# Performance work log

Measured on AMD Instinct MI355X. Metric: run time of the kernel, lower is better.

Reference implementation:

```python
import jax, jax.numpy as jnp
import numpy as np

EMBED_DIM = 1024
B, S = 4, 2048


def setup_inputs() -> dict:
    key = jax.random.key(0)
    ks = jax.random.split(key, 7)
    D = EMBED_DIM
    lim = 1.0 / np.sqrt(D)  # torch nn.Linear default init range
    inp = {
        "input": jax.random.normal(ks[0], (B, S, D), dtype=jnp.float32),
        "Wq": jax.random.uniform(ks[1], (D, D), jnp.float32, -lim, lim),
        "bq": jax.random.uniform(ks[2], (D,), jnp.float32, -lim, lim),
        "Wk": jax.random.uniform(ks[3], (D, D), jnp.float32, -lim, lim),
        "bk": jax.random.uniform(ks[4], (D,), jnp.float32, -lim, lim),
        "Wv": jax.random.uniform(ks[5], (D, D), jnp.float32, -lim, lim),
        "bv": jax.random.uniform(ks[6], (D,), jnp.float32, -lim, lim),
    }
    return inp


def reference(input, Wq, bq, Wk, bk, Wv, bv):
    # Linear layers: x @ W^T + b (torch convention: W is [out, in])
    q = jnp.einsum("bsd,ed->bse", input, Wq) + bq
    k = jnp.einsum("bsd,ed->bse", input, Wk) + bk
    v = jnp.einsum("bsd,ed->bse", input, Wv) + bv
    scale = 1.0 / jnp.sqrt(jnp.float32(EMBED_DIM))
    # [B, S, S] similarity matrix (unfused, matches original)
    similarity = jnp.einsum("bqd,bkd->bqk", q, k) * scale
    attention = jax.nn.softmax(similarity, axis=-1)
    return jnp.einsum("bqk,bkd->bqd", attention, v)
```

## Files before the change

kernel.cpp:

```cpp
#include <hip/hip_runtime.h>


typedef unsigned short ushort_t;
typedef __bf16 bf16x8 __attribute__((ext_vector_type(8)));
typedef float f32x4 __attribute__((ext_vector_type(4)));

__device__ __forceinline__ unsigned short f2bf(float f) {
  unsigned u = __builtin_bit_cast(unsigned, f);
  u += 0x7fffu + ((u >> 16) & 1u);
  return (unsigned short)(u >> 16);
}

template<int BM, int MODE, int RX, int RY>
__global__ __launch_bounds__(512, 1)
void gemm8p(const ushort_t* __restrict__ A, long long sAz, int lda,
            const ushort_t* __restrict__ Bm, long long sBz, int ldb,
            void* __restrict__ C0, void* __restrict__ C1, void* __restrict__ C2,
            long long sCz, int ldc, int K, float scale, const float* __restrict__ bias)
{
  constexpr int MF  = BM / 32;
  constexpr int MH  = MF / 2;
  constexpr int AH  = (BM / 2) * 64;
  constexpr int BH  = 128 * 64;
  constexpr int BUF = 2 * AH + 2 * BH;
  constexpr int SWA = AH / 4096;
  constexpr int BPR = RX * RY;
  __shared__ ushort_t lds_[2 * BUF] __attribute__((aligned(16)));

  const int gx = gridDim.x;
  const int lin = blockIdx.y * gx + blockIdx.x;
  const int xcd = lin & 7, s = lin >> 3;
  const int chunk = s / BPR, idx = s % BPR;
  const int rect = chunk * 8 + xcd;
  const int nrx = gx / RX;
  const int bx = (rect % nrx) * RX + (idx % RX);
  const int by = (rect / nrx) * RY + (idx / RX);

  const int z = blockIdx.z;
  const ushort_t* Ab = A  + (long long)z * sAz + (long long)by * BM  * lda;
  const ushort_t* Bb = Bm + (long long)z * sBz + (long long)bx * 256 * ldb;

  const int tid = threadIdx.x, wid = tid >> 6, lane = tid & 63;
  const int wr = wid >> 2, wc = wid & 3;
  const int l15 = lane & 15;
  const int kx0 = (((lane >> 4) + 0) ^ (l15 & 7)) * 8;
  const int kx1 = (((lane >> 4) + 4) ^ (l15 & 7)) * 8;
  const int srow = lane >> 3;
  const int scol = ((lane & 7) ^ (srow & 7)) * 8;

  auto stgA = [&](int q, int h, int t) {
#pragma unroll
    for (int j = 0; j < SWA; ++j) {
      const ushort_t* g = Ab + (long long)(h * (BM / 2) + wid * (8 * SWA) + j * 8 + srow) * lda
                             + t * 64 + scol;
      __builtin_amdgcn_global_load_lds(
          (const __attribute__((address_space(1))) void*)g,
          (__attribute__((address_space(3))) void*)
            (&lds_[q * BUF + h * AH + (wid * (64 * SWA) + j * 64) * 8]),
          16, 0, 0);
    }
  };
  auto stgB = [&](int q, int h, int t) {
#pragma unroll
    for (int j = 0; j < 2; ++j) {
      const ushort_t* g = Bb + (long long)(h * 128 + wid * 16 + j * 8 + srow) * ldb
                             + t * 64 + scol;
      __builtin_amdgcn_global_load_lds(
          (const __attribute__((address_space(1))) void*)g,
          (__attribute__((address_space(3))) void*)
            (&lds_[q * BUF + 2 * AH + h * BH + (wid * 128 + j * 64) * 8]),
          16, 0, 0);
    }
  };

  f32x4 acc[MF][4];
#pragma unroll
  for (int m = 0; m < MF; ++m)
#pragma unroll
    for (int n = 0; n < 4; ++n)
#pragma unroll
      for (int j = 0; j < 4; ++j) acc[m][n][j] = 0.f;

  stgA(0, 0, 0); stgA(0, 1, 0);
  stgB(0, 0, 0); stgB(0, 1, 0);
  stgA(1, 0, 1); stgA(1, 1, 1);
  if constexpr (SWA == 2) asm volatile("s_waitcnt vmcnt(4)" ::: "memory");
  else                    asm volatile("s_waitcnt vmcnt(2)" ::: "memory");
  __builtin_amdgcn_s_barrier();

  const int NT = K >> 6;

  if constexpr (MF == 4) {
    bf16x8 a0[4], a1[4], bf[4];
    for (int t = 0; t < NT; ++t) {
      const int q = t & 1;
      const ushort_t* Al = &lds_[q * BUF + wr * AH];
      const ushort_t* Bl = &lds_[q * BUF + 2 * AH + (wc >> 1) * BH + (wc & 1) * 4096];

#pragma unroll
      for (int m = 0; m < 4; ++m) a0[m] = *(const bf16x8*)(Al + (m * 16 + l15) * 64 + kx0);
#pragma unroll
      for (int n = 0; n < 4; ++n) bf[n] = *(const bf16x8*)(Bl + (n * 16 + l15) * 64 + kx0);
#pragma unroll
      for (int m = 0; m < 4; ++m) a1[m] = *(const bf16x8*)(Al + (m * 16 + l15) * 64 + kx1);
      __builtin_amdgcn_sched_barrier(0);
      if (t + 1 < NT) { stgB(q ^ 1, 0, t + 1); stgB(q ^ 1, 1, t + 1); }
      __builtin_amdgcn_s_barrier();
      __builtin_amdgcn_s_setprio(1);
#pragma unroll
      for (int m = 0; m < 4; ++m)
#pragma unroll
        for (int n = 0; n < 4; ++n)
          acc[m][n] = __builtin_amdgcn_mfma_f32_16x16x32_bf16(a0[m], bf[n], acc[m][n], 0, 0, 0);
      __builtin_amdgcn_s_setprio(0);
      __builtin_amdgcn_s_barrier();

#pragma unroll
      for (int n = 0; n < 4; ++n) bf[n] = *(const bf16x8*)(Bl + (n * 16 + l15) * 64 + kx1);
      __builtin_amdgcn_sched_barrier(0);
      if (t + 2 < NT) { stgA(q, 0, t + 2); stgA(q, 1, t + 2); }
      __builtin_amdgcn_s_barrier();
      __builtin_amdgcn_s_setprio(1);
#pragma unroll
      for (int m = 0; m < 4; ++m)
#pragma unroll
        for (int n = 0; n < 4; ++n)
          acc[m][n] = __builtin_amdgcn_mfma_f32_16x16x32_bf16(a1[m], bf[n], acc[m][n], 0, 0, 0);
      __builtin_amdgcn_s_setprio(0);
      if (t < NT - 2)       asm volatile("s_waitcnt vmcnt(2)" ::: "memory");
      else if (t == NT - 2) asm volatile("s_waitcnt vmcnt(0)" ::: "memory");
      __builtin_amdgcn_s_barrier();
    }
  } else {
    bf16x8 af[MH], bf[4];
    for (int t = 0; t < NT; ++t) {
      const int q = t & 1;
      const ushort_t* Al = &lds_[q * BUF + wr * AH];
      const ushort_t* Bl = &lds_[q * BUF + 2 * AH + (wc >> 1) * BH + (wc & 1) * 4096];

#pragma unroll
      for (int n = 0; n < 4; ++n) bf[n] = *(const bf16x8*)(Bl + (n * 16 + l15) * 64 + kx0);
#pragma unroll
      for (int m = 0; m < MH; ++m) af[m] = *(const bf16x8*)(Al + (m * 16 + l15) * 64 + kx0);
      if (t + 1 < NT) stgB(q ^ 1, 0, t + 1);
      __builtin_amdgcn_s_barrier();
      __builtin_amdgcn_s_setprio(1);
#pragma unroll
      for (int m = 0; m < MH; ++m)
#pragma unroll
        for (int n = 0; n < 4; ++n)
          acc[m][n] = __builtin_amdgcn_mfma_f32_16x16x32_bf16(af[m], bf[n], acc[m][n], 0, 0, 0);
      __builtin_amdgcn_s_setprio(0);
      __builtin_amdgcn_s_barrier();

#pragma unroll
      for (int m = 0; m < MH; ++m) af[m] = *(const bf16x8*)(Al + ((MH + m) * 16 + l15) * 64 + kx0);
      if (t + 1 < NT) stgB(q ^ 1, 1, t + 1);
      __builtin_amdgcn_s_barrier();
      __builtin_amdgcn_s_setprio(1);
#pragma unroll
      for (int m = 0; m < MH; ++m)
#pragma unroll
        for (int n = 0; n < 4; ++n)
          acc[MH + m][n] = __builtin_amdgcn_mfma_f32_16x16x32_bf16(af[m], bf[n], acc[MH + m][n], 0, 0, 0);
      __builtin_amdgcn_s_setprio(0);
      __builtin_amdgcn_s_barrier();

#pragma unroll
      for (int n = 0; n < 4; ++n) bf[n] = *(const bf16x8*)(Bl + (n * 16 + l15) * 64 + kx1);
#pragma unroll
      for (int m = 0; m < MH; ++m) af[m] = *(const bf16x8*)(Al + (m * 16 + l15) * 64 + kx1);
      __builtin_amdgcn_s_barrier();
      __builtin_amdgcn_s_setprio(1);
#pragma unroll
      for (int m = 0; m < MH; ++m)
#pragma unroll
        for (int n = 0; n < 4; ++n)
          acc[m][n] = __builtin_amdgcn_mfma_f32_16x16x32_bf16(af[m], bf[n], acc[m][n], 0, 0, 0);
      __builtin_amdgcn_s_setprio(0);
      __builtin_amdgcn_s_barrier();

#pragma unroll
      for (int m = 0; m < MH; ++m) af[m] = *(const bf16x8*)(Al + ((MH + m) * 16 + l15) * 64 + kx1);
      __builtin_amdgcn_sched_barrier(0);
      if (t + 2 < NT) { stgA(q, 0, t + 2); stgA(q, 1, t + 2); }
      __builtin_amdgcn_s_barrier();
      __builtin_amdgcn_s_setprio(1);
#pragma unroll
      for (int m = 0; m < MH; ++m)
#pragma unroll
        for (int n = 0; n < 4; ++n)
          acc[MH + m][n] = __builtin_amdgcn_mfma_f32_16x16x32_bf16(af[m], bf[n], acc[MH + m][n], 0, 0, 0);
      __builtin_amdgcn_s_setprio(0);
      if (t < NT - 2)       asm volatile("s_waitcnt vmcnt(4)" ::: "memory");
      else if (t == NT - 2) asm volatile("s_waitcnt vmcnt(0)" ::: "memory");
      __builtin_amdgcn_s_barrier();
    }
  }

  const int r4 = (lane >> 4) * 4;
  const long long crow0 = (long long)by * BM + wr * (BM / 2);
  const int ccol0 = bx * 256 + wc * 64;
#pragma unroll
  for (int n = 0; n < 4; ++n) {
    const int cg = ccol0 + n * 16 + l15;
    const float badd = bias ? bias[cg] : 0.f;
    ushort_t* outp = (ushort_t*)C0;
    int col = cg;
    if constexpr (MODE == 2) {
      const int sel = cg >> 10;
      col = cg & 1023;
      outp = (ushort_t*)(sel == 0 ? C0 : (sel == 1 ? C1 : C2));
    }
#pragma unroll
    for (int m = 0; m < MF; ++m)
#pragma unroll
      for (int j = 0; j < 4; ++j) {
        const long long rg = crow0 + m * 16 + r4 + j;
        const float v = acc[m][n][j] * scale + badd;
        if constexpr (MODE == 0)
          ((float*)C0)[(long long)z * sCz + rg * ldc + cg] = v;
        else if constexpr (MODE == 1)
          ((ushort_t*)C0)[(long long)z * sCz + rg * ldc + cg] = f2bf(v);
        else
          outp[rg * 1024 + col] = f2bf(v);
      }
  }
}

__global__ __launch_bounds__(256)
void cast_f32_bf16(const float* __restrict__ in, ushort_t* __restrict__ out, long long n)
{
  long long i = ((long long)blockIdx.x * blockDim.x + threadIdx.x) * 4;
  const long long stride = (long long)gridDim.x * blockDim.x * 4;
  for (; i < n; i += stride) {
    const float4 v = *(const float4*)&in[i];
    ushort4 o;
    o.x = f2bf(v.x); o.y = f2bf(v.y); o.z = f2bf(v.z); o.w = f2bf(v.w);
    *(ushort4*)&out[i] = o;
  }
}

__global__ __launch_bounds__(256)
void prep_w(const float* __restrict__ Wq, const float* __restrict__ Wk,
            const float* __restrict__ Wv, const float* __restrict__ bq,
            const float* __restrict__ bk, const float* __restrict__ bv,
            ushort_t* __restrict__ w3, float* __restrict__ bcat)
{
  const int which = blockIdx.x >> 10;
  const float* W = (which == 0) ? Wq : (which == 1) ? Wk : Wv;
  const long long i = ((long long)(blockIdx.x & 1023) * 256 + threadIdx.x) * 4;
  const float4 v = *(const float4*)&W[i];
  ushort4 o;
  o.x = f2bf(v.x); o.y = f2bf(v.y); o.z = f2bf(v.z); o.w = f2bf(v.w);
  *(ushort4*)&w3[(long long)which * 1024 * 1024 + i] = o;
  const int g = blockIdx.x * 256 + threadIdx.x;
  if (g < 3072) bcat[g] = (g < 1024) ? bq[g] : (g < 2048) ? bk[g - 1024] : bv[g - 2048];
}

__global__ __launch_bounds__(256)
void transpose_bf16(const ushort_t* __restrict__ in, ushort_t* __restrict__ out,
                    int rows, int cols, int ldIn, long long sIn, long long sOut)
{
  __shared__ ushort_t t[64][65];
  in  += (long long)blockIdx.z * sIn;
  out += (long long)blockIdx.z * sOut;
  const int r0 = blockIdx.y * 64;
  const int c0 = blockIdx.x * 64;
  const int tx = threadIdx.x & 15, ty = threadIdx.x >> 4;
#pragma unroll
  for (int r = 0; r < 4; ++r) {
    const ushort4 v = *(const ushort4*)&in[(long long)(r0 + ty * 4 + r) * ldIn + c0 + tx * 4];
    t[ty * 4 + r][tx * 4 + 0] = v.x;
    t[ty * 4 + r][tx * 4 + 1] = v.y;
    t[ty * 4 + r][tx * 4 + 2] = v.z;
    t[ty * 4 + r][tx * 4 + 3] = v.w;
  }
  __syncthreads();
#pragma unroll
  for (int r = 0; r < 4; ++r) {
    const int d = ty * 4 + r;
    ushort4 v;
    v.x = t[tx * 4 + 0][d];
    v.y = t[tx * 4 + 1][d];
    v.z = t[tx * 4 + 2][d];
    v.w = t[tx * 4 + 3][d];
    *(ushort4*)&out[(long long)(c0 + d) * rows + r0 + tx * 4] = v;
  }
}

__global__ __launch_bounds__(256)
void softmax2048(const float* __restrict__ Sc, ushort_t* __restrict__ P)
{
  const long long row = blockIdx.x;
  const float* s = Sc + row * 2048;
  const int tid = threadIdx.x;
  const int wave = tid >> 6, lane = tid & 63;

  const float4 a = *(const float4*)&s[tid * 4];
  const float4 b = *(const float4*)&s[1024 + tid * 4];
  float m = fmaxf(fmaxf(fmaxf(a.x, a.y), fmaxf(a.z, a.w)),
                  fmaxf(fmaxf(b.x, b.y), fmaxf(b.z, b.w)));
#pragma unroll
  for (int off = 32; off > 0; off >>= 1) m = fmaxf(m, __shfl_xor(m, off));
  __shared__ float redm[4], reds[4];
  if (lane == 0) redm[wave] = m;
  __syncthreads();
  m = fmaxf(fmaxf(redm[0], redm[1]), fmaxf(redm[2], redm[3]));

  float e[8];
  e[0] = __expf(a.x - m); e[1] = __expf(a.y - m); e[2] = __expf(a.z - m); e[3] = __expf(a.w - m);
  e[4] = __expf(b.x - m); e[5] = __expf(b.y - m); e[6] = __expf(b.z - m); e[7] = __expf(b.w - m);
  float sum = ((e[0] + e[1]) + (e[2] + e[3])) + ((e[4] + e[5]) + (e[6] + e[7]));
#pragma unroll
  for (int off = 32; off > 0; off >>= 1) sum += __shfl_xor(sum, off);
  if (lane == 0) reds[wave] = sum;
  __syncthreads();
  sum = (reds[0] + reds[1]) + (reds[2] + reds[3]);
  const float inv = 1.0f / sum;

  ushort4 o;
  o.x = f2bf(e[0] * inv); o.y = f2bf(e[1] * inv); o.z = f2bf(e[2] * inv); o.w = f2bf(e[3] * inv);
  *(ushort4*)&P[row * 2048 + tid * 4] = o;
  o.x = f2bf(e[4] * inv); o.y = f2bf(e[5] * inv); o.z = f2bf(e[6] * inv); o.w = f2bf(e[7] * inv);
  *(ushort4*)&P[row * 2048 + 1024 + tid * 4] = o;
}

extern "C" void kernel_launch(void* const* d_in, const int* in_sizes, int n_in,
                              void* d_out, int out_size, void* d_ws, size_t ws_size,
                              hipStream_t stream)
{
  constexpr int B = 4, S = 2048, D = 1024;
  constexpr long long MT = (long long)B * S;
  constexpr long long SD = (long long)S * D;
  constexpr long long SS = (long long)S * S;

  const float* x  = (const float*)d_in[0];
  const float* Wq = (const float*)d_in[1];
  const float* bq = (const float*)d_in[2];
  const float* Wk = (const float*)d_in[3];
  const float* bk = (const float*)d_in[4];
  const float* Wv = (const float*)d_in[5];
  const float* bv = (const float*)d_in[6];
  float* out = (float*)d_out;

  char* base = (char*)d_ws;
  ushort_t* q      = (ushort_t*)(base);
  ushort_t* k      = (ushort_t*)(base + 16777216);
  ushort_t* vt     = (ushort_t*)(base + 33554432);
  float*    scores = (float*)   (base + 50331648);
  ushort_t* P      = (ushort_t*)(base + 117440512);
  ushort_t* vplain = (ushort_t*)(base + 150994944);
  ushort_t* xb     = (ushort_t*)(base + 50331648);
  ushort_t* w3     = (ushort_t*)(base + 67108864);
  float*    bcat   = (float*)   (base + 73400320);

  cast_f32_bf16<<<2048, 256, 0, stream>>>(x, xb, MT * D);
  prep_w<<<3072, 256, 0, stream>>>(Wq, Wk, Wv, bq, bk, bv, w3, bcat);

  gemm8p<128, 2, 4, 8><<<dim3(12, 64, 1), 512, 0, stream>>>(
      xb, 0, D, w3, 0, D, q, k, vplain, 0, 1024, D, 1.f, bcat);

  transpose_bf16<<<dim3(16, 32, 4), 256, 0, stream>>>(
      vplain, vt, S, D, 1024, SD, SD);

  gemm8p<256, 0, 4, 2><<<dim3(8, 8, 4), 512, 0, stream>>>(
      q, SD, D, k, SD, D, scores, nullptr, nullptr, SS, S, D, 0.03125f, nullptr);

  softmax2048<<<MT, 256, 0, stream>>>(scores, P);

  gemm8p<128, 0, 2, 4><<<dim3(4, 16, 4), 512, 0, stream>>>(
      P, SS, S, vt, (long long)D * S, S, out, nullptr, nullptr, SD, D, S, 1.f, nullptr);
}
```

Measured before the change: 185.0 us.

## Fuse V transpose into QKV GEMM epilogue and use 128x128 tiles with higher occupancy

Splits the templated GEMM into a 128x128-tile kernel (launch bounds allowing 4 blocks per CU) and a dedicated 256x256 kernel for the QK^T scores. The QKV projection GEMM now writes the V slice directly in transposed layout from its epilogue, which removes the separate transpose kernel and the extra round trip through memory. The QKV and PV GEMMs move to smaller tiles with more blocks, trading per-block reuse for better occupancy and wave coverage. The transposed V stores are 8-byte strided writes, which may coalesce worse than the old row-major stores.

Result: faster. 175.8 us (-5.0%).

```diff
diff --git a/kernel.cpp b/kernel.cpp
--- a/kernel.cpp
+++ b/kernel.cpp
@@ -11,22 +11,18 @@
   return (unsigned short)(u >> 16);
 }
 
-template<int BM, int MODE, int RX, int RY>
-__global__ __launch_bounds__(512, 1)
-void gemm8p(const ushort_t* __restrict__ A, long long sAz, int lda,
-            const ushort_t* __restrict__ Bm, long long sBz, int ldb,
-            void* __restrict__ C0, void* __restrict__ C1, void* __restrict__ C2,
-            long long sCz, int ldc, int K, float scale, const float* __restrict__ bias)
-{
-  constexpr int MF  = BM / 32;
-  constexpr int MH  = MF / 2;
-  constexpr int AH  = (BM / 2) * 64;
-  constexpr int BH  = 128 * 64;
-  constexpr int BUF = 2 * AH + 2 * BH;
-  constexpr int SWA = AH / 4096;
+template<int MODE, int RX, int RY>
+__global__ __launch_bounds__(512, 4)
+void gemm128(const ushort_t* __restrict__ A, long long sAz, int lda,
+             const ushort_t* __restrict__ Bm, long long sBz, int ldb,
+             void* __restrict__ C0, void* __restrict__ C1, void* __restrict__ C2,
+             long long sCz, int ldc, int K, float scale, const float* __restrict__ bias)
+{
+  constexpr int SLOT = 8192;
+  constexpr int BUF  = 2 * SLOT;
+  __shared__ ushort_t lds_[2 * BUF] __attribute__((aligned(16)));
+
   constexpr int BPR = RX * RY;
-  __shared__ ushort_t lds_[2 * BUF] __attribute__((aligned(16)));
-
   const int gx = gridDim.x;
   const int lin = blockIdx.y * gx + blockIdx.x;
   const int xcd = lin & 7, s = lin >> 3;
@@ -37,8 +33,8 @@
   const int by = (rect / nrx) * RY + (idx / RX);
 
   const int z = blockIdx.z;
-  const ushort_t* Ab = A  + (long long)z * sAz + (long long)by * BM  * lda;
-  const ushort_t* Bb = Bm + (long long)z * sBz + (long long)bx * 256 * ldb;
+  const ushort_t* Ab = A  + (long long)z * sAz + (long long)by * 128 * lda;
+  const ushort_t* Bb = Bm + (long long)z * sBz + (long long)bx * 128 * ldb;
 
   const int tid = threadIdx.x, wid = tid >> 6, lane = tid & 63;
   const int wr = wid >> 2, wc = wid & 3;
@@ -48,15 +44,165 @@
   const int srow = lane >> 3;
   const int scol = ((lane & 7) ^ (srow & 7)) * 8;
 
+  auto stg = [&](int mat, int q, int t) {
+    const ushort_t* g0 = (mat == 0 ? Ab : Bb);
+    const int ld = (mat == 0 ? lda : ldb);
+#pragma unroll
+    for (int j = 0; j < 2; ++j) {
+      const ushort_t* g = g0 + (long long)(j * 64 + wid * 8 + srow) * ld + t * 64 + scol;
+      __builtin_amdgcn_global_load_lds(
+          (const __attribute__((address_space(1))) void*)g,
+          (__attribute__((address_space(3))) void*)
+            (&lds_[q * BUF + mat * SLOT + (j * 64 + wid * 8) * 64]),
+          16, 0, 0);
+    }
+  };
+
+  f32x4 acc[4][2];
+#pragma unroll
+  for (int m = 0; m < 4; ++m)
+#pragma unroll
+    for (int n = 0; n < 2; ++n)
+#pragma unroll
+      for (int j = 0; j < 4; ++j) acc[m][n][j] = 0.f;
+
+  stg(0, 0, 0); stg(1, 0, 0); stg(0, 1, 1);
+  asm volatile("s_waitcnt vmcnt(2)" ::: "memory");
+  __builtin_amdgcn_s_barrier();
+
+  const int NT = K >> 6;
+  bf16x8 a0[4], a1[4], bf[2];
+
+  for (int t = 0; t < NT; ++t) {
+    const int q = t & 1;
+    const ushort_t* Al = &lds_[q * BUF] + wr * 64 * 64;
+    const ushort_t* Bl = &lds_[q * BUF + SLOT] + wc * 32 * 64;
+
+#pragma unroll
+    for (int m = 0; m < 4; ++m) a0[m] = *(const bf16x8*)(Al + (m * 16 + l15) * 64 + kx0);
+#pragma unroll
+    for (int n = 0; n < 2; ++n) bf[n] = *(const bf16x8*)(Bl + (n * 16 + l15) * 64 + kx0);
+#pragma unroll
+    for (int m = 0; m < 4; ++m) a1[m] = *(const bf16x8*)(Al + (m * 16 + l15) * 64 + kx1);
+    __builtin_amdgcn_sched_barrier(0);
+    if (t + 1 < NT) stg(1, q ^ 1, t + 1);
+    __builtin_amdgcn_s_barrier();
+    __builtin_amdgcn_s_setprio(1);
+#pragma unroll
+    for (int m = 0; m < 4; ++m)
+#pragma unroll
+      for (int n = 0; n < 2; ++n)
+        acc[m][n] = __builtin_amdgcn_mfma_f32_16x16x32_bf16(a0[m], bf[n], acc[m][n], 0, 0, 0);
+    __builtin_amdgcn_s_setprio(0);
+    __builtin_amdgcn_s_barrier();
+
+#pragma unroll
+    for (int n = 0; n < 2; ++n) bf[n] = *(const bf16x8*)(Bl + (n * 16 + l15) * 64 + kx1);
+    __builtin_amdgcn_sched_barrier(0);
+    if (t + 2 < NT) stg(0, q, t + 2);
+    __builtin_amdgcn_s_barrier();
+    __builtin_amdgcn_s_setprio(1);
+#pragma unroll
+    for (int m = 0; m < 4; ++m)
+#pragma unroll
+      for (int n = 0; n < 2; ++n)
+        acc[m][n] = __builtin_amdgcn_mfma_f32_16x16x32_bf16(a1[m], bf[n], acc[m][n], 0, 0, 0);
+    __builtin_amdgcn_s_setprio(0);
+    if (t < NT - 2)       asm volatile("s_waitcnt vmcnt(2)" ::: "memory");
+    else if (t == NT - 2) asm volatile("s_waitcnt vmcnt(0)" ::: "memory");
+    __builtin_amdgcn_s_barrier();
+  }
+
+  const int r4 = (lane >> 4) * 4;
+  const long long crow0 = (long long)by * 128 + wr * 64;
+  const int ccol0 = bx * 128 + wc * 32;
+
+  if constexpr (MODE == 0) {
+#pragma unroll
+    for (int n = 0; n < 2; ++n) {
+      const int cg = ccol0 + n * 16 + l15;
+#pragma unroll
+      for (int m = 0; m < 4; ++m)
+#pragma unroll
+        for (int j = 0; j < 4; ++j) {
+          const long long rg = crow0 + m * 16 + r4 + j;
+          ((float*)C0)[(long long)z * sCz + rg * ldc + cg] = acc[m][n][j] * scale;
+        }
+    }
+  } else {
+    const int sel = ccol0 >> 10;
+#pragma unroll
+    for (int n = 0; n < 2; ++n) {
+      const int cg = ccol0 + n * 16 + l15;
+      const int col = cg & 1023;
+      const float badd = bias[cg];
+      if (sel < 2) {
+        ushort_t* outp = (ushort_t*)(sel == 0 ? C0 : C1);
+#pragma unroll
+        for (int m = 0; m < 4; ++m)
+#pragma unroll
+          for (int j = 0; j < 4; ++j) {
+            const long long rg = crow0 + m * 16 + r4 + j;
+            outp[rg * 1024 + col] = f2bf(acc[m][n][j] + badd);
+          }
+      } else {
+        ushort_t* vt = (ushort_t*)C2;
+#pragma unroll
+        for (int m = 0; m < 4; ++m) {
+          const long long rg = crow0 + m * 16 + r4;
+          const long long b = rg >> 11, srw = rg & 2047;
+          ushort4 o;
+          o.x = f2bf(acc[m][n][0] + badd);
+          o.y = f2bf(acc[m][n][1] + badd);
+          o.z = f2bf(acc[m][n][2] + badd);
+          o.w = f2bf(acc[m][n][3] + badd);
+          *(ushort4*)&vt[b * 2097152 + (long long)col * 2048 + srw] = o;
+        }
+      }
+    }
+  }
+}
+
+__global__ __launch_bounds__(512, 1)
+void gemm256(const ushort_t* __restrict__ A, long long sAz, int lda,
+             const ushort_t* __restrict__ Bm, long long sBz, int ldb,
+             float* __restrict__ C, long long sCz, int ldc,
+             int K, float scale)
+{
+  constexpr int AH = 8192, BH = 8192, BUF = 2 * AH + 2 * BH;
+  constexpr int RX = 4, RY = 2, BPR = RX * RY;
+  __shared__ ushort_t lds_[2 * BUF] __attribute__((aligned(16)));
+
+  const int gx = gridDim.x;
+  const int lin = blockIdx.y * gx + blockIdx.x;
+  const int xcd = lin & 7, s = lin >> 3;
+  const int chunk = s / BPR, idx = s % BPR;
+  const int rect = chunk * 8 + xcd;
+  const int nrx = gx / RX;
+  const int bx = (rect % nrx) * RX + (idx % RX);
+  const int by = (rect / nrx) * RY + (idx / RX);
+
+  const int z = blockIdx.z;
+  const ushort_t* Ab = A  + (long long)z * sAz + (long long)by * 256 * lda;
+  const ushort_t* Bb = Bm + (long long)z * sBz + (long long)bx * 256 * ldb;
+
+  const int tid = threadIdx.x, wid = tid >> 6, lane = tid & 63;
+  const int wr = wid >> 2, wc = wid & 3;
+  const int l15 = lane & 15;
+  const int kx0 = (((lane >> 4) + 0) ^ (l15 & 7)) * 8;
+  const int kx1 = (((lane >> 4) + 4) ^ (l15 & 7)) * 8;
+  const int srow = lane >> 3;
+  const int scol = ((lane & 7) ^ (srow & 7)) * 8;
+
   auto stgA = [&](int q, int h, int t) {
 #pragma unroll
-    for (int j = 0; j < SWA; ++j) {
-      const ushort_t* g = Ab + (long long)(h * (BM / 2) + wid * (8 * SWA) + j * 8 + srow) * lda
+    for (int j = 0; j < 2; ++j) {
+      const ushort_t* g = Ab + (long long)(h * 128 + wid * 16 + j * 8 + srow) * lda
                              + t * 64 + scol;
       __builtin_amdgcn_global_load_lds(
           (const __attribute__((address_space(1))) void*)g,
           (__attribute__((address_space(3))) void*)
-            (&lds_[q * BUF + h * AH + (wid * (64 * SWA) + j * 64) * 8]),
+            (&lds_[q * BUF + h * AH + (wid * 128 + j * 64) * 8]),
           16, 0, 0);
     }
   };
@@ -73,9 +219,9 @@
     }
   };
 
-  f32x4 acc[MF][4];
-#pragma unroll
-  for (int m = 0; m < MF; ++m)
+  f32x4 acc[8][4];
+#pragma unroll
+  for (int m = 0; m < 8; ++m)
 #pragma unroll
     for (int n = 0; n < 4; ++n)
 #pragma unroll
@@ -84,146 +230,88 @@
   stgA(0, 0, 0); stgA(0, 1, 0);
   stgB(0, 0, 0); stgB(0, 1, 0);
   stgA(1, 0, 1); stgA(1, 1, 1);
-  if constexpr (SWA == 2) asm volatile("s_waitcnt vmcnt(4)" ::: "memory");
-  else                    asm volatile("s_waitcnt vmcnt(2)" ::: "memory");
+  asm volatile("s_waitcnt vmcnt(4)" ::: "memory");
   __builtin_amdgcn_s_barrier();
 
   const int NT = K >> 6;
-
-  if constexpr (MF == 4) {
-    bf16x8 a0[4], a1[4], bf[4];
-    for (int t = 0; t < NT; ++t) {
-      const int q = t & 1;
-      const ushort_t* Al = &lds_[q * BUF + wr * AH];
-      const ushort_t* Bl = &lds_[q * BUF + 2 * AH + (wc >> 1) * BH + (wc & 1) * 4096];
-
-#pragma unroll
-      for (int m = 0; m < 4; ++m) a0[m] = *(const bf16x8*)(Al + (m * 16 + l15) * 64 + kx0);
-#pragma unroll
-      for (int n = 0; n < 4; ++n) bf[n] = *(const bf16x8*)(Bl + (n * 16 + l15) * 64 + kx0);
-#pragma unroll
-      for (int m = 0; m < 4; ++m) a1[m] = *(const bf16x8*)(Al + (m * 16 + l15) * 64 + kx1);
-      __builtin_amdgcn_sched_barrier(0);
-      if (t + 1 < NT) { stgB(q ^ 1, 0, t + 1); stgB(q ^ 1, 1, t + 1); }
-      __builtin_amdgcn_s_barrier();
-      __builtin_amdgcn_s_setprio(1);
-#pragma unroll
-      for (int m = 0; m < 4; ++m)
-#pragma unroll
-        for (int n = 0; n < 4; ++n)
-          acc[m][n] = __builtin_amdgcn_mfma_f32_16x16x32_bf16(a0[m], bf[n], acc[m][n], 0, 0, 0);
-      __builtin_amdgcn_s_setprio(0);
-      __builtin_amdgcn_s_barrier();
-
-#pragma unroll
-      for (int n = 0; n < 4; ++n) bf[n] = *(const bf16x8*)(Bl + (n * 16 + l15) * 64 + kx1);
-      __builtin_amdgcn_sched_barrier(0);
-      if (t + 2 < NT) { stgA(q, 0, t + 2); stgA(q, 1, t + 2); }
-      __builtin_amdgcn_s_barrier();
-      __builtin_amdgcn_s_setprio(1);
-#pragma unroll
-      for (int m = 0; m < 4; ++m)
-#pragma unroll
-        for (int n = 0; n < 4; ++n)
-          acc[m][n] = __builtin_amdgcn_mfma_f32_16x16x32_bf16(a1[m], bf[n], acc[m][n], 0, 0, 0);
-      __builtin_amdgcn_s_setprio(0);
-      if (t < NT - 2)       asm volatile("s_waitcnt vmcnt(2)" ::: "memory");
-      else if (t == NT - 2) asm volatile("s_waitcnt vmcnt(0)" ::: "memory");
-      __builtin_amdgcn_s_barrier();
-    }
-  } else {
-    bf16x8 af[MH], bf[4];
-    for (int t = 0; t < NT; ++t) {
-      const int q = t & 1;
-      const ushort_t* Al = &lds_[q * BUF + wr * AH];
-      const ushort_t* Bl = &lds_[q * BUF + 2 * AH + (wc >> 1) * BH + (wc & 1) * 4096];
-
-#pragma unroll
-      for (int n = 0; n < 4; ++n) bf[n] = *(const bf16x8*)(Bl + (n * 16 + l15) * 64 + kx0);
-#pragma unroll
-      for (int m = 0; m < MH; ++m) af[m] = *(const bf16x8*)(Al + (m * 16 + l15) * 64 + kx0);
-      if (t + 1 < NT) stgB(q ^ 1, 0, t + 1);
-      __builtin_amdgcn_s_barrier();
-      __builtin_amdgcn_s_setprio(1);
-#pragma unroll
-      for (int m = 0; m < MH; ++m)
-#pragma unroll
-        for (int n = 0; n < 4; ++n)
-          acc[m][n] = __builtin_amdgcn_mfma_f32_16x16x32_bf16(af[m], bf[n], acc[m][n], 0, 0, 0);
-      __builtin_amdgcn_s_setprio(0);
-      __builtin_amdgcn_s_barrier();
-
-#pragma unroll
-      for (int m = 0; m < MH; ++m) af[m] = *(const bf16x8*)(Al + ((MH + m) * 16 + l15) * 64 + kx0);
-      if (t + 1 < NT) stgB(q ^ 1, 1, t + 1);
-      __builtin_amdgcn_s_barrier();
-      __builtin_amdgcn_s_setprio(1);
-#pragma unroll
-      for (int m = 0; m < MH; ++m)
-#pragma unroll
-        for (int n = 0; n < 4; ++n)
-          acc[MH + m][n] = __builtin_amdgcn_mfma_f32_16x16x32_bf16(af[m], bf[n], acc[MH + m][n], 0, 0, 0);
-      __builtin_amdgcn_s_setprio(0);
-      __builtin_amdgcn_s_barrier();
-
-#pragma unroll
-      for (int n = 0; n < 4; ++n) bf[n] = *(const bf16x8*)(Bl + (n * 16 + l15) * 64 + kx1);
-#pragma unroll
-      for (int m = 0; m < MH; ++m) af[m] = *(const bf16x8*)(Al + (m * 16 + l15) * 64 + kx1);
-      __builtin_amdgcn_s_barrier();
-      __builtin_amdgcn_s_setprio(1);
-#pragma unroll
-      for (int m = 0; m < MH; ++m)
-#pragma unroll
-        for (int n = 0; n < 4; ++n)
-          acc[m][n] = __builtin_amdgcn_mfma_f32_16x16x32_bf16(af[m], bf[n], acc[m][n], 0, 0, 0);
-      __builtin_amdgcn_s_setprio(0);
-      __builtin_amdgcn_s_barrier();
-
-#pragma unroll
-      for (int m = 0; m < MH; ++m) af[m] = *(const bf16x8*)(Al + ((MH + m) * 16 + l15) * 64 + kx1);
-      __builtin_amdgcn_sched_barrier(0);
-      if (t + 2 < NT) { stgA(q, 0, t + 2); stgA(q, 1, t + 2); }
-      __builtin_amdgcn_s_barrier();
-      __builtin_amdgcn_s_setprio(1);
-#pragma unroll
-      for (int m = 0; m < MH; ++m)
-#pragma unroll
-        for (int n = 0; n < 4; ++n)
-          acc[MH + m][n] = __builtin_amdgcn_mfma_f32_16x16x32_bf16(af[m], bf[n], acc[MH + m][n], 0, 0, 0);
-      __builtin_amdgcn_s_setprio(0);
-      if (t < NT - 2)       asm volatile("s_waitcnt vmcnt(4)" ::: "memory");
-      else if (t == NT - 2) asm volatile("s_waitcnt vmcnt(0)" ::: "memory");
-      __builtin_amdgcn_s_barrier();
-    }
+  bf16x8 af[4], bf[4];
+
+  for (int t = 0; t < NT; ++t) {
+    const int q = t & 1;
+    const ushort_t* Al = &lds_[q * BUF + wr * AH];
+    const ushort_t* Bl = &lds_[q * BUF + 2 * AH + (wc >> 1) * BH + (wc & 1) * 4096];
+
+#pragma unroll
+    for (int n = 0; n < 4; ++n) bf[n] = *(const bf16x8*)(Bl + (n * 16 + l15) * 64 + kx0);
+#pragma unroll
+    for (int m = 0; m < 4; ++m) af[m] = *(const bf16x8*)(Al + (m * 16 + l15) * 64 + kx0);
+    if (t + 1 < NT) stgB(q ^ 1, 0, t + 1);
+    __builtin_amdgcn_s_barrier();
+    __builtin_amdgcn_s_setprio(1);
+#pragma unroll
+    for (int m = 0; m < 4; ++m)
+#pragma unroll
+      for (int n = 0; n < 4; ++n)
+        acc[m][n] = __builtin_amdgcn_mfma_f32_16x16x32_bf16(af[m], bf[n], acc[m][n], 0, 0, 0);
+    __builtin_amdgcn_s_setprio(0);
+    __builtin_amdgcn_s_barrier();
+
+#pragma unroll
+    for (int m = 0; m < 4; ++m) af[m] = *(const bf16x8*)(Al + ((4 + m) * 16 + l15) * 64 + kx0);
+    if (t + 1 < NT) stgB(q ^ 1, 1, t + 1);
+    __builtin_amdgcn_s_barrier();
+    __builtin_amdgcn_s_setprio(1);
+#pragma unroll
+    for (int m = 0; m < 4; ++m)
+#pragma unroll
+      for (int n = 0; n < 4; ++n)
+        acc[4 + m][n] = __builtin_amdgcn_mfma_f32_16x16x32_bf16(af[m], bf[n], acc[4 + m][n], 0, 0, 0);
+    __builtin_amdgcn_s_setprio(0);
+    __builtin_amdgcn_s_barrier();
+
+#pragma unroll
+    for (int n = 0; n < 4; ++n) bf[n] = *(const bf16x8*)(Bl + (n * 16 + l15) * 64 + kx1);
+#pragma unroll
+    for (int m = 0; m < 4; ++m) af[m] = *(const bf16x8*)(Al + (m * 16 + l15) * 64 + kx1);
+    __builtin_amdgcn_s_barrier();
+    __builtin_amdgcn_s_setprio(1);
+#pragma unroll
+    for (int m = 0; m < 4; ++m)
+#pragma unroll
+      for (int n = 0; n < 4; ++n)
+        acc[m][n] = __builtin_amdgcn_mfma_f32_16x16x32_bf16(af[m], bf[n], acc[m][n], 0, 0, 0);
+    __builtin_amdgcn_s_setprio(0);
+    __builtin_amdgcn_s_barrier();
+
+#pragma unroll
+    for (int m = 0; m < 4; ++m) af[m] = *(const bf16x8*)(Al + ((4 + m) * 16 + l15) * 64 + kx1);
+    __builtin_amdgcn_sched_barrier(0);
+    if (t + 2 < NT) { stgA(q, 0, t + 2); stgA(q, 1, t + 2); }
+    __builtin_amdgcn_s_barrier();
+    __builtin_amdgcn_s_setprio(1);
+#pragma unroll
+    for (int m = 0; m < 4; ++m)
+#pragma unroll
+      for (int n = 0; n < 4; ++n)
+        acc[4 + m][n] = __builtin_amdgcn_mfma_f32_16x16x32_bf16(af[m], bf[n], acc[4 + m][n], 0, 0, 0);
+    __builtin_amdgcn_s_setprio(0);
+    if (t < NT - 2)       asm volatile("s_waitcnt vmcnt(4)" ::: "memory");
+    else if (t == NT - 2) asm volatile("s_waitcnt vmcnt(0)" ::: "memory");
+    __builtin_amdgcn_s_barrier();
   }
 
   const int r4 = (lane >> 4) * 4;
-  const long long crow0 = (long long)by * BM + wr * (BM / 2);
+  const long long crow0 = (long long)by * 256 + wr * 128;
   const int ccol0 = bx * 256 + wc * 64;
 #pragma unroll
   for (int n = 0; n < 4; ++n) {
     const int cg = ccol0 + n * 16 + l15;
-    const float badd = bias ? bias[cg] : 0.f;
-    ushort_t* outp = (ushort_t*)C0;
-    int col = cg;
-    if constexpr (MODE == 2) {
-      const int sel = cg >> 10;
-      col = cg & 1023;
-      outp = (ushort_t*)(sel == 0 ? C0 : (sel == 1 ? C1 : C2));
-    }
-#pragma unroll
-    for (int m = 0; m < MF; ++m)
+#pragma unroll
+    for (int m = 0; m < 8; ++m)
 #pragma unroll
       for (int j = 0; j < 4; ++j) {
         const long long rg = crow0 + m * 16 + r4 + j;
-        const float v = acc[m][n][j] * scale + badd;
-        if constexpr (MODE == 0)
-          ((float*)C0)[(long long)z * sCz + rg * ldc + cg] = v;
-        else if constexpr (MODE == 1)
-          ((ushort_t*)C0)[(long long)z * sCz + rg * ldc + cg] = f2bf(v);
-        else
-          outp[rg * 1024 + col] = f2bf(v);
+        C[(long long)z * sCz + rg * ldc + cg] = acc[m][n][j] * scale;
       }
   }
 }
@@ -259,37 +347,6 @@
 }
 
 __global__ __launch_bounds__(256)
-void transpose_bf16(const ushort_t* __restrict__ in, ushort_t* __restrict__ out,
-                    int rows, int cols, int ldIn, long long sIn, long long sOut)
-{
-  __shared__ ushort_t t[64][65];
-  in  += (long long)blockIdx.z * sIn;
-  out += (long long)blockIdx.z * sOut;
-  const int r0 = blockIdx.y * 64;
-  const int c0 = blockIdx.x * 64;
-  const int tx = threadIdx.x & 15, ty = threadIdx.x >> 4;
-#pragma unroll
-  for (int r = 0; r < 4; ++r) {
-    const ushort4 v = *(const ushort4*)&in[(long long)(r0 + ty * 4 + r) * ldIn + c0 + tx * 4];
-    t[ty * 4 + r][tx * 4 + 0] = v.x;
-    t[ty * 4 + r][tx * 4 + 1] = v.y;
-    t[ty * 4 + r][tx * 4 + 2] = v.z;
-    t[ty * 4 + r][tx * 4 + 3] = v.w;
-  }
-  __syncthreads();
-#pragma unroll
-  for (int r = 0; r < 4; ++r) {
-    const int d = ty * 4 + r;
-    ushort4 v;
-    v.x = t[tx * 4 + 0][d];
-    v.y = t[tx * 4 + 1][d];
-    v.z = t[tx * 4 + 2][d];
-    v.w = t[tx * 4 + 3][d];
-    *(ushort4*)&out[(long long)(c0 + d) * rows + r0 + tx * 4] = v;
-  }
-}
-
-__global__ __launch_bounds__(256)
 void softmax2048(const float* __restrict__ Sc, ushort_t* __restrict__ P)
 {
   const long long row = blockIdx.x;
@@ -350,7 +407,6 @@
   ushort_t* vt     = (ushort_t*)(base + 33554432);
   float*    scores = (float*)   (base + 50331648);
   ushort_t* P      = (ushort_t*)(base + 117440512);
-  ushort_t* vplain = (ushort_t*)(base + 150994944);
   ushort_t* xb     = (ushort_t*)(base + 50331648);
   ushort_t* w3     = (ushort_t*)(base + 67108864);
   float*    bcat   = (float*)   (base + 73400320);
@@ -358,17 +414,14 @@
   cast_f32_bf16<<<2048, 256, 0, stream>>>(x, xb, MT * D);
   prep_w<<<3072, 256, 0, stream>>>(Wq, Wk, Wv, bq, bk, bv, w3, bcat);
 
-  gemm8p<128, 2, 4, 8><<<dim3(12, 64, 1), 512, 0, stream>>>(
-      xb, 0, D, w3, 0, D, q, k, vplain, 0, 1024, D, 1.f, bcat);
-
-  transpose_bf16<<<dim3(16, 32, 4), 256, 0, stream>>>(
-      vplain, vt, S, D, 1024, SD, SD);
-
-  gemm8p<256, 0, 4, 2><<<dim3(8, 8, 4), 512, 0, stream>>>(
-      q, SD, D, k, SD, D, scores, nullptr, nullptr, SS, S, D, 0.03125f, nullptr);
+  gemm128<2, 4, 8><<<dim3(24, 64, 1), 512, 0, stream>>>(
+      xb, 0, D, w3, 0, D, q, k, vt, 0, 1024, D, 1.f, bcat);
+
+  gemm256<<<dim3(8, 8, 4), 512, 0, stream>>>(
+      q, SD, D, k, SD, D, scores, SS, S, D, 0.03125f);
 
   softmax2048<<<MT, 256, 0, stream>>>(scores, P);
 
-  gemm8p<128, 0, 2, 4><<<dim3(4, 16, 4), 512, 0, stream>>>(
+  gemm128<0, 2, 4><<<dim3(8, 16, 4), 512, 0, stream>>>(
       P, SS, S, vt, (long long)D * S, S, out, nullptr, nullptr, SD, D, S, 1.f, nullptr);
 }
```
